# Performance work log

Measured on AMD Instinct MI355X. Metric: run time of the kernel, lower is better.

Reference implementation:

```python
import jax, jax.numpy as jnp
from jax import lax
import numpy as np

# Problem dims (from init_kwargs / input_specs)
B, NC, NX, NY = 16, 31, 256, 256   # cube: batch, spectral channels, spatial
NO, KX, KY = 3, 17, 17             # diffraction orders, kernel spatial size
PAD = 4                            # findclusters dilation padding
N_LOC = NO * NC * (2 * PAD + 1) ** 2  # 7533 trainable kernel entries


def _build_locations():
    """Emulate findclusters: one dispersion delta per (order, channel),
    dilated by a (2*PAD+1)^2 window. Returns flat int32 indices into
    the flattened (NO, NC, KX, KY) kernel."""
    idxs = []
    cy = KX // 2  # 8
    lo, hi = PAD, KX - 1 - PAD  # valid center range [4, 12]
    for o in range(NO):
        for c in range(NC):
            # channel-dependent horizontal dispersion, order-dependent sign
            shift = (o - 1) * (c * PAD * 2 // (NC - 1))
            cx = int(np.clip(cy + shift, lo, hi))
            for dy in range(-PAD, PAD + 1):
                for dx in range(-PAD, PAD + 1):
                    idxs.append(((o * NC + c) * KX + (cy + dy)) * KY + (cx + dx))
    return jnp.asarray(np.array(idxs, dtype=np.int32))


def setup_inputs() -> dict:
    key = jax.random.key(0)
    k1, k2 = jax.random.split(key)
    x = jax.random.normal(k1, (B, NC, NX, NY), dtype=jnp.float32)
    # trainable sparse kernel values (mostly positive so ReLU passes most)
    variable_kernel = jax.random.uniform(k2, (N_LOC,), dtype=jnp.float32,
                                         minval=-0.2, maxval=1.0)
    locations = _build_locations()
    return {"x": x, "variable_kernel": variable_kernel, "locations": locations}


def reference(x, variable_kernel, locations):
    # fill_kernel: scatter ReLU'd trainable values into a zero kernel
    kernel = (jnp.zeros((NO * NC * KX * KY,), x.dtype)
              .at[locations].set(jax.nn.relu(variable_kernel))
              .reshape(NO, NC, KX, KY))
    # disperse_all_orders: per-order dispersion conv, summed over spectral
    # channels -> measurement per order. out: (B, NO, NX, NY)
    out = lax.conv_general_dilated(
        x, kernel, window_strides=(1, 1), padding="SAME",
        dimension_numbers=("NCHW", "OIHW", "NCHW"))
    return out
```

## Files before the change

### kernel.cpp

```cpp
#include <hip/hip_runtime.h>

namespace {

constexpr int kB  = 16;
constexpr int kNC = 31;
constexpr int kNX = 256;
constexpr int kNY = 256;
constexpr int kNO = 3;
constexpr int kKS = 17;

constexpr int TX = 64;
constexpr int TY = 32;
constexpr int HTX = TX + 16;
constexpr int HTY = TY + 8;
constexpr int XPITCH = 81;
constexpr int WPITCH = 12;
constexpr int NOC = kNO * kNC;

__global__ __launch_bounds__(256, 2)
void disperse_conv(const float* __restrict__ x,
                   const float* __restrict__ vk,
                   const int* __restrict__ loc,
                   float* __restrict__ out)
{
    __shared__ __align__(16) float wlds[NOC * 9 * WPITCH];
    __shared__ __align__(16) float xtile[HTY * XPITCH];
    __shared__ int sol[NOC];

    const int tid = threadIdx.x;
    const int x0 = blockIdx.x * TX;
    const int y0 = blockIdx.y * TY;
    const int b  = blockIdx.z;

    for (int i = tid; i < NOC * 9 * WPITCH; i += 256) {
        int dx = i % WPITCH;
        int rowi = i / WPITCH;
        float v = 0.0f;
        if (dx < 9) {
            float t = vk[rowi * 9 + dx];
            v = t > 0.0f ? t : 0.0f;
        }
        wlds[i] = v;
    }
    if (tid < NOC) {
        int l0 = loc[tid * 81];
        int cx = l0 - (tid * kKS + 4) * kKS + 4;
        sol[tid] = cx - 4;
    }

    const int tx = tid & 7;
    const int ty = tid >> 3;
    const int xo = tx * 8;

    float acc[kNO][8];
    #pragma unroll
    for (int o = 0; o < kNO; ++o)
        #pragma unroll
        for (int j = 0; j < 8; ++j)
            acc[o][j] = 0.0f;

    for (int c = 0; c < kNC; ++c) {
        __syncthreads();
        const float* xc = x + (size_t)(b * kNC + c) * kNX * kNY;
        for (int i = tid; i < HTY * (HTX / 4); i += 256) {
            int r  = i / (HTX / 4);
            int cv = (i - r * (HTX / 4)) * 4;
            int gy = y0 - 4 + r;
            int gx = x0 - 8 + cv;
            float4 v = make_float4(0.f, 0.f, 0.f, 0.f);
            if ((unsigned)gy < (unsigned)kNX && (unsigned)gx < (unsigned)kNY)
                v = *(const float4*)(xc + (size_t)gy * kNY + gx);
            float* d = &xtile[r * XPITCH + cv];
            d[0] = v.x; d[1] = v.y; d[2] = v.z; d[3] = v.w;
        }
        __syncthreads();

        #pragma unroll
        for (int o = 0; o < kNO; ++o) {
            const int oc = o * kNC + c;
            const int so = sol[oc];
            const float* wbase = &wlds[oc * 9 * WPITCH];
            #pragma unroll 1
            for (int dy = 0; dy < 9; ++dy) {
                const float* xt = &xtile[(ty + dy) * XPITCH + xo + so];
                float xr[16];
                #pragma unroll
                for (int i = 0; i < 16; ++i) xr[i] = xt[i];
                const float4* wv = (const float4*)(wbase + dy * WPITCH);
                float4 w0 = wv[0], w1 = wv[1], w2 = wv[2];
                float w[9] = {w0.x, w0.y, w0.z, w0.w, w1.x, w1.y, w1.z, w1.w, w2.x};
                #pragma unroll
                for (int dx = 0; dx < 9; ++dx)
                    #pragma unroll
                    for (int j = 0; j < 8; ++j)
                        acc[o][j] = fmaf(w[dx], xr[j + dx], acc[o][j]);
            }
        }
    }

    #pragma unroll
    for (int o = 0; o < kNO; ++o) {
        size_t base = (((size_t)b * kNO + o) * kNX + (size_t)(y0 + ty)) * kNY
                      + (size_t)(x0 + xo);
        *(float4*)(out + base)     = make_float4(acc[o][0], acc[o][1], acc[o][2], acc[o][3]);
        *(float4*)(out + base + 4) = make_float4(acc[o][4], acc[o][5], acc[o][6], acc[o][7]);
    }
}

}

extern "C" void kernel_launch(void* const* d_in, const int* in_sizes, int n_in,
                              void* d_out, int out_size, void* d_ws, size_t ws_size,
                              hipStream_t stream)
{
    const float* x  = (const float*)d_in[0];
    const float* vk = (const float*)d_in[1];
    const int* loc  = (const int*)d_in[2];
    float* out = (float*)d_out;

    dim3 grid(kNY / TX, kNX / TY, kB);
    dim3 block(256);
    hipLaunchKernelGGL(disperse_conv, grid, block, 0, stream, x, vk, loc, out);
}
```

Before: 522.9 us.

## Precompute ReLU weights in prep kernel, share row loads across orders, switch-dispatch shifts

Moves the ReLU'd weight table and per-(order, channel) shift computation into a separate prep kernel writing to workspace, so each conv block no longer rebuilds them in LDS. The conv kernel now loads one 24-wide row of the input tile with float4 LDS reads per dy and reuses it across all three orders. A switch over the shift value selects a register window at compile time. Weights are read through global/scalar memory, LDS use drops, and launch bounds target 4 blocks per CU. The trade-offs are an extra kernel launch, possible register pressure from the 24-element buffer plus switch code, and weights no longer coming from LDS.

```diff
diff --git a/kernel.cpp b/kernel.cpp
--- a/kernel.cpp
+++ b/kernel.cpp
@@ -8,45 +8,54 @@
 constexpr int kNY = 256;
 constexpr int kNO = 3;
 constexpr int kKS = 17;
+constexpr int NOC = kNO * kNC;
 
 constexpr int TX = 64;
 constexpr int TY = 32;
-constexpr int HTX = TX + 16;
 constexpr int HTY = TY + 8;
-constexpr int XPITCH = 81;
-constexpr int WPITCH = 12;
-constexpr int NOC = kNO * kNC;
+constexpr int XP  = 84;
+constexpr int WROW = 16;
 
-__global__ __launch_bounds__(256, 2)
+__global__ void prep(const float* __restrict__ vk, const int* __restrict__ loc,
+                     float* __restrict__ wrel, int* __restrict__ soTab)
+{
+    int i = blockIdx.x * 256 + threadIdx.x;
+    if (i < NOC * 9 * WROW) {
+        int dx  = i & 15;
+        int row = i >> 4;
+        float v = 0.0f;
+        if (dx < 9) {
+            float t = vk[row * 9 + dx];
+            v = t > 0.0f ? t : 0.0f;
+        }
+        wrel[i] = v;
+    }
+    if (i < NOC) {
+        int cx = loc[i * 81] - (i * kKS + 4) * kKS + 4;
+        soTab[i] = cx - 4;
+    }
+}
+
+template<int S>
+__device__ __forceinline__ void extract16(float* __restrict__ xr,
+                                          const float* __restrict__ xu)
+{
+    #pragma unroll
+    for (int i = 0; i < 16; ++i) xr[i] = xu[i + S];
+}
+
+__global__ __launch_bounds__(256, 4)
 void disperse_conv(const float* __restrict__ x,
-                   const float* __restrict__ vk,
-                   const int* __restrict__ loc,
+                   const float* __restrict__ wrel,
+                   const int* __restrict__ soTab,
                    float* __restrict__ out)
 {
-    __shared__ __align__(16) float wlds[NOC * 9 * WPITCH];
-    __shared__ __align__(16) float xtile[HTY * XPITCH];
-    __shared__ int sol[NOC];
+    __shared__ __align__(16) float xtile[HTY * XP];
 
     const int tid = threadIdx.x;
     const int x0 = blockIdx.x * TX;
     const int y0 = blockIdx.y * TY;
     const int b  = blockIdx.z;
-
-    for (int i = tid; i < NOC * 9 * WPITCH; i += 256) {
-        int dx = i % WPITCH;
-        int rowi = i / WPITCH;
-        float v = 0.0f;
-        if (dx < 9) {
-            float t = vk[rowi * 9 + dx];
-            v = t > 0.0f ? t : 0.0f;
-        }
-        wlds[i] = v;
-    }
-    if (tid < NOC) {
-        int l0 = loc[tid * 81];
-        int cx = l0 - (tid * kKS + 4) * kKS + 4;
-        sol[tid] = cx - 4;
-    }
 
     const int tx = tid & 7;
     const int ty = tid >> 3;
@@ -62,38 +71,61 @@
     for (int c = 0; c < kNC; ++c) {
         __syncthreads();
         const float* xc = x + (size_t)(b * kNC + c) * kNX * kNY;
-        for (int i = tid; i < HTY * (HTX / 4); i += 256) {
-            int r  = i / (HTX / 4);
-            int cv = (i - r * (HTX / 4)) * 4;
-            int gy = y0 - 4 + r;
-            int gx = x0 - 8 + cv;
-            float4 v = make_float4(0.f, 0.f, 0.f, 0.f);
-            if ((unsigned)gy < (unsigned)kNX && (unsigned)gx < (unsigned)kNY)
-                v = *(const float4*)(xc + (size_t)gy * kNY + gx);
-            float* d = &xtile[r * XPITCH + cv];
-            d[0] = v.x; d[1] = v.y; d[2] = v.z; d[3] = v.w;
+        #pragma unroll
+        for (int it = 0; it < 4; ++it) {
+            int i = it * 256 + tid;
+            if (i < HTY * 20) {
+                int r = i / 20;
+                int k = i - r * 20;
+                int gy = y0 - 4 + r;
+                int gx = x0 - 8 + k * 4;
+                float4 v = make_float4(0.f, 0.f, 0.f, 0.f);
+                if ((unsigned)gy < (unsigned)kNX && (unsigned)gx < (unsigned)kNY)
+                    v = *(const float4*)(xc + (size_t)gy * kNY + gx);
+                *(float4*)&xtile[r * XP + k * 4] = v;
+            }
         }
         __syncthreads();
 
-        #pragma unroll
-        for (int o = 0; o < kNO; ++o) {
-            const int oc = o * kNC + c;
-            const int so = sol[oc];
-            const float* wbase = &wlds[oc * 9 * WPITCH];
-            #pragma unroll 1
-            for (int dy = 0; dy < 9; ++dy) {
-                const float* xt = &xtile[(ty + dy) * XPITCH + xo + so];
+        const int so0 = soTab[0 * kNC + c];
+        const int so1 = soTab[1 * kNC + c];
+        const int so2 = soTab[2 * kNC + c];
+
+        #pragma unroll 1
+        for (int dy = 0; dy < 9; ++dy) {
+            float xu[24];
+            const float* srow = &xtile[(ty + dy) * XP + xo];
+            #pragma unroll
+            for (int k2 = 0; k2 < 6; ++k2)
+                *(float4*)&xu[k2 * 4] = *(const float4*)&srow[k2 * 4];
+
+            #pragma unroll
+            for (int o = 0; o < kNO; ++o) {
+                const int oc = o * kNC + c;
+                const int so = (o == 0) ? so0 : (o == 1) ? so1 : so2;
+                const float* wr = &wrel[(oc * 9 + dy) * WROW];
+                float w[9];
+                #pragma unroll
+                for (int d = 0; d < 9; ++d) w[d] = wr[d];
+
                 float xr[16];
+                switch (so) {
+                    case 0: extract16<0>(xr, xu); break;
+                    case 1: extract16<1>(xr, xu); break;
+                    case 2: extract16<2>(xr, xu); break;
+                    case 3: extract16<3>(xr, xu); break;
+                    case 4: extract16<4>(xr, xu); break;
+                    case 5: extract16<5>(xr, xu); break;
+                    case 6: extract16<6>(xr, xu); break;
+                    case 7: extract16<7>(xr, xu); break;
+                    default: extract16<8>(xr, xu); break;
+                }
+
                 #pragma unroll
-                for (int i = 0; i < 16; ++i) xr[i] = xt[i];
-                const float4* wv = (const float4*)(wbase + dy * WPITCH);
-                float4 w0 = wv[0], w1 = wv[1], w2 = wv[2];
-                float w[9] = {w0.x, w0.y, w0.z, w0.w, w1.x, w1.y, w1.z, w1.w, w2.x};
-                #pragma unroll
-                for (int dx = 0; dx < 9; ++dx)
+                for (int d = 0; d < 9; ++d)
                     #pragma unroll
                     for (int j = 0; j < 8; ++j)
-                        acc[o][j] = fmaf(w[dx], xr[j + dx], acc[o][j]);
+                        acc[o][j] = fmaf(w[d], xr[j + d], acc[o][j]);
             }
         }
     }
@@ -116,9 +148,15 @@
     const float* x  = (const float*)d_in[0];
     const float* vk = (const float*)d_in[1];
     const int* loc  = (const int*)d_in[2];
-    float* out = (float*)d_out;
+    float* outp = (float*)d_out;
+
+    float* wrel = (float*)d_ws;
+    int*   soTab = (int*)(wrel + NOC * 9 * WROW);
+
+    dim3 pgrid((NOC * 9 * WROW + 255) / 256);
+    hipLaunchKernelGGL(prep, pgrid, dim3(256), 0, stream, vk, loc, wrel, soTab);
 
     dim3 grid(kNY / TX, kNX / TY, kB);
-    dim3 block(256);
-    hipLaunchKernelGGL(disperse_conv, grid, block, 0, stream, x, vk, loc, out);
+    hipLaunchKernelGGL(disperse_conv, grid, dim3(256), 0, stream,
+                       x, wrel, soTab, outp);
 }
```

Result: slower. 726.2 us (+38.9%).
